# Optimization experiments

Measured on AMD Instinct MI355X. Metric: run time of the kernel, lower is better.

## Reference

```python
import jax, jax.numpy as jnp
import numpy as np

N_NODES = 100000
N_EDGES = 1600000
IN_F, HID, OUT_F = 64, 64, 64
NUM_RELS, NUM_BASES = 4, 2


def _glorot(key, shape):
    fan_in, fan_out = shape[-2], shape[-1]
    lim = jnp.sqrt(6.0 / (fan_in + fan_out))
    return jax.random.uniform(key, shape, jnp.float32, -lim, lim)


def setup_inputs() -> dict:
    key = jax.random.key(0)
    ks = jax.random.split(key, 16)
    inp = {
        "features": jax.random.normal(ks[0], (N_NODES, IN_F), jnp.float32),
        "src": jax.random.randint(ks[1], (N_EDGES,), 0, N_NODES, jnp.int32),
        "dst": jax.random.randint(ks[2], (N_EDGES,), 0, N_NODES, jnp.int32),
        "edge_types": jax.random.randint(ks[3], (N_EDGES,), 0, NUM_RELS, jnp.int32),
    }
    dims = [(IN_F, HID), (HID, HID), (HID, OUT_F)]
    for i, (di, do) in enumerate(dims, start=1):
        inp[f"bases{i}"] = _glorot(ks[3 + 3 * i], (NUM_BASES, di, do))
        inp[f"comp{i}"] = _glorot(ks[4 + 3 * i], (NUM_RELS, NUM_BASES))
        inp[f"loop_w{i}"] = _glorot(ks[5 + 3 * i], (di, do))
        inp[f"bias{i}"] = jnp.zeros((do,), jnp.float32)
    inp["pred_w"] = _glorot(ks[13], (OUT_F, 1))
    inp["pred_b"] = jnp.zeros((1,), jnp.float32)
    return inp


def rel_graph_conv(x, src, dst, etypes, bases, comp, loop_w, bias):
    # basis-composed per-node transform: [N, B, out]
    xb = jnp.einsum('ni,bio->nbo', x, bases)
    # per-edge message: combine basis outputs of source node with comp[etype]
    msg = jnp.einsum('eb,ebo->eo', comp[etypes], xb[src])  # [E, out]
    agg = jax.ops.segment_sum(msg, dst, num_segments=x.shape[0])
    return agg + x @ loop_w + bias


def reference(features, src, dst, edge_types,
              bases1, comp1, loop_w1, bias1,
              bases2, comp2, loop_w2, bias2,
              bases3, comp3, loop_w3, bias3,
              pred_w, pred_b):
    x = jax.nn.relu(rel_graph_conv(features, src, dst, edge_types, bases1, comp1, loop_w1, bias1))
    # dropout is identity in eval mode
    x = jax.nn.relu(rel_graph_conv(x, src, dst, edge_types, bases2, comp2, loop_w2, bias2))
    x = jax.nn.relu(rel_graph_conv(x, src, dst, edge_types, bases3, comp3, loop_w3, bias3))
    logits = (x @ pred_w + pred_b)[:, 0]
    return jax.nn.sigmoid(logits)
```

## Files before the change

### kernel.cpp

```cpp
#include <hip/hip_runtime.h>
#include <hip/hip_bf16.h>
#include <hip/hip_fp16.h>


#define NB1 196
#define NBLK1 256
#define BUCKET_SHIFT 9
#define PAD_ALLOW 4096
#define WT_LD 200
#define DUMMY_PK (4 << 17)
#define WNODES 8

typedef unsigned short ushort_t;
typedef _Float16 h8 __attribute__((ext_vector_type(8)));
typedef float f32x4 __attribute__((ext_vector_type(4)));

__device__ inline ushort_t f2h(float f) {
  __half h = __float2half_rn(f);
  return *(ushort_t*)&h;
}
__device__ inline float h2f(ushort_t u) {
  __half h = *(__half*)&u;
  return __half2float(h);
}

__device__ inline int block_incl_scan_256(int v, int* wsums) {
  int lane = threadIdx.x & 63, wid = threadIdx.x >> 6;
  int s = v;
#pragma unroll
  for (int off = 1; off < 64; off <<= 1) {
    int u = __shfl_up(s, off, 64);
    if (lane >= off) s += u;
  }
  if (lane == 63) wsums[wid] = s;
  __syncthreads();
  if (threadIdx.x == 0) {
    int a = 0;
#pragma unroll
    for (int w = 0; w < 4; ++w) { int t = wsums[w]; wsums[w] = a; a += t; }
  }
  __syncthreads();
  return s + wsums[wid];
}

__global__ void __launch_bounds__(256) k_l1hist(const int* __restrict__ dst,
                                                int* __restrict__ H, int E, int chunk) {
  __shared__ int h[NB1];
  int t = threadIdx.x;
  if (t < NB1) h[t] = 0;
  __syncthreads();
  int beg = blockIdx.x * chunk;
  int end = min(beg + chunk, E);
  for (int i = beg + t; i < end; i += 256) atomicAdd(&h[dst[i] >> BUCKET_SHIFT], 1);
  __syncthreads();
  if (t < NB1) H[blockIdx.x * NB1 + t] = h[t];
}

__global__ void __launch_bounds__(256) k_colscan(int* __restrict__ H,
                                                 int* __restrict__ total) {
  __shared__ int wsums[4];
  int b = blockIdx.x;
  int t = threadIdx.x;
  int v = H[t * NB1 + b];
  int s = block_incl_scan_256(v, wsums);
  H[t * NB1 + b] = s - v;
  if (t == 255) total[b] = s;
}

__global__ void __launch_bounds__(256) k_basescan(const int* __restrict__ total,
                                                  int* __restrict__ bucket_base) {
  __shared__ int wsums[4];
  int t = threadIdx.x;
  int v = (t < NB1) ? total[t] : 0;
  int s = block_incl_scan_256(v, wsums);
  if (t < NB1) bucket_base[t] = s - v;
  if (t == 255) bucket_base[NB1] = s;
}

__global__ void __launch_bounds__(256) k_scatter1(
    const int* __restrict__ src, const int* __restrict__ dst,
    const int* __restrict__ et, const int* __restrict__ H,
    const int* __restrict__ bucket_base, int* __restrict__ epk1,
    int E, int chunk) {
  __shared__ int cur[NB1];
  int t = threadIdx.x;
  if (t < NB1) cur[t] = bucket_base[t] + H[blockIdx.x * NB1 + t];
  __syncthreads();
  int beg = blockIdx.x * chunk;
  int end = min(beg + chunk, E);
  for (int i = beg + t; i < end; i += 256) {
    int d = dst[i];
    int b = d >> BUCKET_SHIFT;
    int p = atomicAdd(&cur[b], 1);
    epk1[p] = src[i] | (et[i] << 17) | ((d & 511) << 20);
  }
}

__global__ void __launch_bounds__(256) k_bucket(
    const int* __restrict__ epk1, const int* __restrict__ bucket_base,
    int* __restrict__ epk, int* __restrict__ row_off,
    int* __restrict__ row_end, int N) {
  __shared__ int hist[512];
  __shared__ int cur[512];
  __shared__ int wsums[4];
  int b = blockIdx.x;
  int t = threadIdx.x;
  int ebase = bucket_base[b], eend = bucket_base[b + 1];
  int pb = ebase + b * PAD_ALLOW;
  hist[t] = 0; hist[t + 256] = 0;
  __syncthreads();
  for (int i = ebase + t; i < eend; i += 256) atomicAdd(&hist[epk1[i] >> 20], 1);
  __syncthreads();
  int h0 = hist[2 * t], h1 = hist[2 * t + 1];
  int pd0 = (h0 == 0) ? 8 : ((h0 + 7) & ~7);
  int pd1 = (h1 == 0) ? 8 : ((h1 + 7) & ~7);
  int pair = pd0 + pd1;
  int incl = block_incl_scan_256(pair, wsums);
  int pe0 = incl - pair;
  int s0 = pb + pe0, s1 = pb + pe0 + pd0;
  cur[2 * t] = s0;
  cur[2 * t + 1] = s1;
  int n0 = (b << BUCKET_SHIFT) + 2 * t;
  if (n0 < N)     { row_off[n0] = s0;     row_end[n0] = s0 + pd0; }
  if (n0 + 1 < N) { row_off[n0 + 1] = s1; row_end[n0 + 1] = s1 + pd1; }
  for (int p = s0 + h0; p < s0 + pd0; ++p) epk[p] = DUMMY_PK;
  for (int p = s1 + h1; p < s1 + pd1; ++p) epk[p] = DUMMY_PK;
  __syncthreads();
  for (int i = ebase + t; i < eend; i += 256) {
    int pk = epk1[i];
    int p = atomicAdd(&cur[pk >> 20], 1);
    epk[p] = pk;
  }
}

__global__ void __launch_bounds__(256) k_quant(const float* __restrict__ in,
                                               ushort_t* __restrict__ out, int n4) {
  int i = blockIdx.x * blockDim.x + threadIdx.x;
  if (i < n4) {
    float4 v = ((const float4*)in)[i];
    ushort4 q;
    q.x = f2h(v.x); q.y = f2h(v.y);
    q.z = f2h(v.z); q.w = f2h(v.w);
    ((ushort4*)out)[i] = q;
  }
}

__global__ void __launch_bounds__(256) k_aggregate(
    const ushort_t* __restrict__ xq, const int* __restrict__ row_off,
    const int* __restrict__ row_end, const int* __restrict__ epk,
    const float* __restrict__ comp, ushort_t* __restrict__ Zh, int N) {
  __shared__ float s_comp[10];
  if (threadIdx.x < 10)
    s_comp[threadIdx.x] = (threadIdx.x < 8) ? comp[threadIdx.x] : 0.f;
  __syncthreads();
  int lane = threadIdx.x & 63;
  int wnode0 = (blockIdx.x * 4 + (threadIdx.x >> 6)) * WNODES;
  if (wnode0 >= N) return;
  int wnode1 = min(wnode0 + WNODES, N);

  int nj = wnode0;
  int ej = row_off[nj], ejEnd = row_end[nj];

  int pkA[8], pkB[8];
  ushort_t xvA[8], xvB[8];
  int nodeA = wnode0, nodeB = wnode0;

#define ISSUE(PK, XV, NODE)                                                 \
  {                                                                         \
    NODE = nj;                                                              \
    _Pragma("unroll") for (int u = 0; u < 8; ++u) PK[u] = epk[ej + u];      \
    _Pragma("unroll") for (int u = 0; u < 8; ++u)                           \
        XV[u] = xq[(size_t)(PK[u] & 0x1FFFF) * 64 + lane];                  \
    ej += 8;                                                                \
    if (ej >= ejEnd) {                                                      \
      if (nj + 1 < wnode1) { ++nj; ej = row_off[nj]; ejEnd = row_end[nj]; } \
      else nj = -1;                                                         \
    }                                                                       \
  }

  int ncons = wnode0;
  float z0 = 0.f, z1 = 0.f;

#define CONSUME(PK, XV, NODE)                                               \
  {                                                                         \
    if (NODE != ncons) {                                                    \
      Zh[(size_t)ncons * 128 + lane] = f2h(z0);                             \
      Zh[(size_t)ncons * 128 + 64 + lane] = f2h(z1);                        \
      z0 = 0.f; z1 = 0.f; ncons = NODE;                                     \
    }                                                                       \
    _Pragma("unroll") for (int u = 0; u < 8; ++u) {                         \
      int r = (PK[u] >> 17) & 7;                                            \
      float xf = h2f(XV[u]);                                                \
      z0 = fmaf(s_comp[r * 2 + 0], xf, z0);                                 \
      z1 = fmaf(s_comp[r * 2 + 1], xf, z1);                                 \
    }                                                                       \
  }

  ISSUE(pkA, xvA, nodeA);
  for (;;) {
    bool haveB = (nj >= 0);
    if (haveB) ISSUE(pkB, xvB, nodeB);
    CONSUME(pkA, xvA, nodeA);
    if (!haveB) break;
    bool haveA = (nj >= 0);
    if (haveA) ISSUE(pkA, xvA, nodeA);
    CONSUME(pkB, xvB, nodeB);
    if (!haveA) break;
  }
  Zh[(size_t)ncons * 128 + lane] = f2h(z0);
  Zh[(size_t)ncons * 128 + 64 + lane] = f2h(z1);
#undef ISSUE
#undef CONSUME
}

__global__ void __launch_bounds__(256) k_gemm_mfma(
    const ushort_t* __restrict__ Zh, const ushort_t* __restrict__ xq,
    const float* __restrict__ bases, const float* __restrict__ loopw,
    const float* __restrict__ bias, ushort_t* __restrict__ xqOut,
    const float* __restrict__ pw, const float* __restrict__ pb,
    float* __restrict__ predOut, int N) {
  __shared__ ushort_t sWh[64 * WT_LD];
  __shared__ ushort_t sWr[64 * WT_LD];
  int t = threadIdx.x;
  int w = t >> 6, l = t & 63;
  int lr = l & 15, lg = l >> 4;
  int row0 = blockIdx.x * 64 + w * 16;

  int arow = row0 + lr;
  bool rok = arow < N;
  h8 a[6];
#pragma unroll
  for (int kb = 0; kb < 6; ++kb) {
    int k0 = kb * 32 + lg * 8;
    uint4 u = make_uint4(0, 0, 0, 0);
    if (rok) {
      if (kb < 4) u = *(const uint4*)(Zh + (size_t)arow * 128 + k0);
      else        u = *(const uint4*)(xq + (size_t)arow * 64 + (k0 - 128));
    }
    a[kb] = *(h8*)&u;
  }

#pragma unroll 4
  for (int i = 0; i < 48; ++i) {
    int idx = i * 256 + t;
    int k = idx >> 6, c = idx & 63;
    float wv = (k < 128) ? bases[idx] : loopw[idx - 8192];
    ushort_t hh = f2h(wv);
    sWh[c * WT_LD + k] = hh;
    sWr[c * WT_LD + k] = f2h(wv - h2f(hh));
  }
  __syncthreads();

  f32x4 acc[4];
#pragma unroll
  for (int c = 0; c < 4; ++c) acc[c] = (f32x4){0.f, 0.f, 0.f, 0.f};
#pragma unroll
  for (int c = 0; c < 4; ++c) {
    int col = c * 16 + lr;
    const ushort_t* bh = sWh + col * WT_LD + lg * 8;
    const ushort_t* br = sWr + col * WT_LD + lg * 8;
#pragma unroll
    for (int kb = 0; kb < 6; ++kb) {
      h8 vb = *(const h8*)(bh + kb * 32);
      acc[c] = __builtin_amdgcn_mfma_f32_16x16x32_f16(a[kb], vb, acc[c], 0, 0, 0);
      h8 vr = *(const h8*)(br + kb * 32);
      acc[c] = __builtin_amdgcn_mfma_f32_16x16x32_f16(a[kb], vr, acc[c], 0, 0, 0);
    }
  }

  float o_[4][4];
#pragma unroll
  for (int c = 0; c < 4; ++c) {
    float bv = bias[c * 16 + lr];
#pragma unroll
    for (int r = 0; r < 4; ++r) o_[c][r] = fmaxf(acc[c][r] + bv, 0.f);
  }
  if (xqOut) {
#pragma unroll
    for (int c = 0; c < 4; ++c) {
      int col = c * 16 + lr;
#pragma unroll
      for (int r = 0; r < 4; ++r) {
        int grow = row0 + lg * 4 + r;
        if (grow < N)
          xqOut[(size_t)grow * 64 + col] = f2h(o_[c][r]);
      }
    }
  }
  if (predOut) {
    float pwv[4];
#pragma unroll
    for (int c = 0; c < 4; ++c) pwv[c] = pw[c * 16 + lr];
#pragma unroll
    for (int r = 0; r < 4; ++r) {
      float s_ = o_[0][r] * pwv[0] + o_[1][r] * pwv[1] +
                 o_[2][r] * pwv[2] + o_[3][r] * pwv[3];
#pragma unroll
      for (int off = 1; off < 16; off <<= 1) s_ += __shfl_xor(s_, off, 64);
      int grow = row0 + lg * 4 + r;
      if (lr == 0 && grow < N) {
        float logit = s_ + pb[0];
        predOut[grow] = 1.f / (1.f + expf(-logit));
      }
    }
  }
}

extern "C" void kernel_launch(void* const* d_in, const int* in_sizes, int n_in,
                              void* d_out, int out_size, void* d_ws, size_t ws_size,
                              hipStream_t stream) {
  const float* features = (const float*)d_in[0];
  const int* src = (const int*)d_in[1];
  const int* dst = (const int*)d_in[2];
  const int* et  = (const int*)d_in[3];
  const float* bases[3] = {(const float*)d_in[4], (const float*)d_in[8],  (const float*)d_in[12]};
  const float* comp[3]  = {(const float*)d_in[5], (const float*)d_in[9],  (const float*)d_in[13]};
  const float* loopw[3] = {(const float*)d_in[6], (const float*)d_in[10], (const float*)d_in[14]};
  const float* biasp[3] = {(const float*)d_in[7], (const float*)d_in[11], (const float*)d_in[15]};
  const float* pred_w = (const float*)d_in[16];
  const float* pred_b = (const float*)d_in[17];

  const int N = in_sizes[0] / 64;
  const int E = in_sizes[1];

  char* ws = (char*)d_ws;
  size_t off = 0;
  auto take = [&](size_t bytes) {
    char* p = ws + off;
    off += (bytes + 255) & ~(size_t)255;
    return p;
  };
  int*      row_off     = (int*)     take((size_t)(N + 1) * 4);
  int*      row_end     = (int*)     take((size_t)N * 4);
  int*      H           = (int*)     take((size_t)NBLK1 * NB1 * 4);
  int*      total       = (int*)     take((size_t)NB1 * 4);
  int*      bucket_base = (int*)     take((size_t)(NB1 + 1) * 4);
  int*      epk         = (int*)     take((size_t)(E + NB1 * PAD_ALLOW + 8) * 4);
  ushort_t* Zh          = (ushort_t*)take((size_t)N * 128 * 2);
  ushort_t* xqA         = (ushort_t*)take((size_t)N * 64 * 2);
  ushort_t* xqB         = (ushort_t*)take((size_t)N * 64 * 2);
  int*      epk1        = (int*)Zh;
  (void)ws_size;

  int chunk = (E + NBLK1 - 1) / NBLK1;
  k_l1hist  <<<NBLK1, 256, 0, stream>>>(dst, H, E, chunk);
  k_colscan <<<NB1,   256, 0, stream>>>(H, total);
  k_basescan<<<1,     256, 0, stream>>>(total, bucket_base);
  k_scatter1<<<NBLK1, 256, 0, stream>>>(src, dst, et, H, bucket_base, epk1, E, chunk);
  k_bucket  <<<NB1,   256, 0, stream>>>(epk1, bucket_base, epk, row_off, row_end, N);

  k_quant<<<(N * 16 + 255) / 256, 256, 0, stream>>>(features, xqA, N * 16);

  ushort_t* bufs[2] = {xqA, xqB};
  int agg_grid = (N + 4 * WNODES - 1) / (4 * WNODES);
  int gemm_grid = (N + 63) / 64;
  for (int l = 0; l < 3; ++l) {
    k_aggregate<<<agg_grid, 256, 0, stream>>>(bufs[l & 1], row_off, row_end,
                                              epk, comp[l], Zh, N);
    bool last = (l == 2);
    k_gemm_mfma<<<gemm_grid, 256, 0, stream>>>(
        Zh, bufs[l & 1], bases[l], loopw[l], biasp[l],
        last ? nullptr : bufs[(l + 1) & 1],
        pred_w, pred_b, last ? (float*)d_out : nullptr, N);
  }
}
```

Baseline: 276.6 us.

## Split edge-packet fetch from gather into a three-stage software pipeline in aggregate

The aggregation kernel now loads the packed edge indices one batch ahead of the feature gather, rotating through three register buffers. The index-load latency is meant to overlap with the previous gather and the accumulation instead of sitting in front of the dependent gather. The relation coefficients are also stored as float2 so each edge needs one LDS read instead of two. This raises register pressure (an extra 8 ints and 8 halves per lane), which could reduce occupancy.

```diff
diff --git a/kernel.cpp b/kernel.cpp
--- a/kernel.cpp
+++ b/kernel.cpp
@@ -149,9 +149,13 @@
     const ushort_t* __restrict__ xq, const int* __restrict__ row_off,
     const int* __restrict__ row_end, const int* __restrict__ epk,
     const float* __restrict__ comp, ushort_t* __restrict__ Zh, int N) {
-  __shared__ float s_comp[10];
-  if (threadIdx.x < 10)
-    s_comp[threadIdx.x] = (threadIdx.x < 8) ? comp[threadIdx.x] : 0.f;
+  __shared__ float2 s_comp[5];
+  if (threadIdx.x < 5) {
+    float2 c2;
+    c2.x = (threadIdx.x < 4) ? comp[threadIdx.x * 2 + 0] : 0.f;
+    c2.y = (threadIdx.x < 4) ? comp[threadIdx.x * 2 + 1] : 0.f;
+    s_comp[threadIdx.x] = c2;
+  }
   __syncthreads();
   int lane = threadIdx.x & 63;
   int wnode0 = (blockIdx.x * 4 + (threadIdx.x >> 6)) * WNODES;
@@ -161,21 +165,25 @@
   int nj = wnode0;
   int ej = row_off[nj], ejEnd = row_end[nj];
 
-  int pkA[8], pkB[8];
-  ushort_t xvA[8], xvB[8];
-  int nodeA = wnode0, nodeB = wnode0;
-
-#define ISSUE(PK, XV, NODE)                                                 \
+  int pkA[8], pkB[8], pkC[8];
+  ushort_t xvA[8], xvB[8], xvC[8];
+  int nodeA = wnode0, nodeB = wnode0, nodeC = wnode0;
+
+#define PKFETCH(PK, NODE)                                                   \
   {                                                                         \
     NODE = nj;                                                              \
     _Pragma("unroll") for (int u = 0; u < 8; ++u) PK[u] = epk[ej + u];      \
-    _Pragma("unroll") for (int u = 0; u < 8; ++u)                           \
-        XV[u] = xq[(size_t)(PK[u] & 0x1FFFF) * 64 + lane];                  \
     ej += 8;                                                                \
     if (ej >= ejEnd) {                                                      \
       if (nj + 1 < wnode1) { ++nj; ej = row_off[nj]; ejEnd = row_end[nj]; } \
       else nj = -1;                                                         \
     }                                                                       \
+  }
+
+#define GATHER(PK, XV)                                                      \
+  {                                                                         \
+    _Pragma("unroll") for (int u = 0; u < 8; ++u)                           \
+        XV[u] = xq[(size_t)(PK[u] & 0x1FFFF) * 64 + lane];                  \
   }
 
   int ncons = wnode0;
@@ -189,27 +197,39 @@
       z0 = 0.f; z1 = 0.f; ncons = NODE;                                     \
     }                                                                       \
     _Pragma("unroll") for (int u = 0; u < 8; ++u) {                         \
-      int r = (PK[u] >> 17) & 7;                                            \
+      float2 cp = s_comp[(PK[u] >> 17) & 7];                                \
       float xf = h2f(XV[u]);                                                \
-      z0 = fmaf(s_comp[r * 2 + 0], xf, z0);                                 \
-      z1 = fmaf(s_comp[r * 2 + 1], xf, z1);                                 \
+      z0 = fmaf(cp.x, xf, z0);                                              \
+      z1 = fmaf(cp.y, xf, z1);                                              \
     }                                                                       \
   }
 
-  ISSUE(pkA, xvA, nodeA);
+  PKFETCH(pkA, nodeA);
+  bool haveB = (nj >= 0);
+  if (haveB) PKFETCH(pkB, nodeB);
+  GATHER(pkA, xvA);
+  bool haveA = true, haveC = false;
   for (;;) {
-    bool haveB = (nj >= 0);
-    if (haveB) ISSUE(pkB, xvB, nodeB);
+    haveC = (nj >= 0);
+    if (haveC) PKFETCH(pkC, nodeC);
+    if (haveB) GATHER(pkB, xvB);
     CONSUME(pkA, xvA, nodeA);
     if (!haveB) break;
-    bool haveA = (nj >= 0);
-    if (haveA) ISSUE(pkA, xvA, nodeA);
+    haveA = (nj >= 0);
+    if (haveA) PKFETCH(pkA, nodeA);
+    if (haveC) GATHER(pkC, xvC);
     CONSUME(pkB, xvB, nodeB);
+    if (!haveC) break;
+    haveB = (nj >= 0);
+    if (haveB) PKFETCH(pkB, nodeB);
+    if (haveA) GATHER(pkA, xvA);
+    CONSUME(pkC, xvC, nodeC);
     if (!haveA) break;
   }
   Zh[(size_t)ncons * 128 + lane] = f2h(z0);
   Zh[(size_t)ncons * 128 + 64 + lane] = f2h(z1);
-#undef ISSUE
+#undef PKFETCH
+#undef GATHER
 #undef CONSUME
 }
 
```

After: 289.7 us. 1.05x slower.
